# Performance work log

Measured on AMD Instinct MI355X. Metric: run time of the kernel, lower is better.

The kernel has to match this reference:

```python
import jax, jax.numpy as jnp
import numpy as np

B, N, IN_C, HID_C, OUT_C = 8, 2048, 128, 256, 32


def setup_inputs() -> dict:
    key = jax.random.key(0)
    ks = jax.random.split(key, 8)
    s1 = 1.0 / np.sqrt(IN_C)
    s2 = 1.0 / np.sqrt(HID_C)
    return {
        "x": jax.random.normal(ks[0], (B, N, IN_C), dtype=jnp.float32),
        "A": jax.random.randint(ks[1], (B, N, N), 0, 2, dtype=jnp.int32),
        "W1_l": jax.random.normal(ks[2], (IN_C, HID_C), dtype=jnp.float32) * s1,
        "W1_r": jax.random.normal(ks[3], (IN_C, HID_C), dtype=jnp.float32) * s1,
        "b1": jnp.zeros((HID_C,), dtype=jnp.float32),
        "W2_l": jax.random.normal(ks[4], (HID_C, OUT_C), dtype=jnp.float32) * s2,
        "W2_r": jax.random.normal(ks[5], (HID_C, OUT_C), dtype=jnp.float32) * s2,
        "b2": jnp.zeros((OUT_C,), dtype=jnp.float32),
    }


def _mean_agg(mask, deg_inv, h):
    # edge (i, j) means source i -> target j (PyG source_to_target flow):
    # agg[b, j] = mean over i with A[b, i, j] != 0 of h[b, i]
    return jnp.einsum("bij,bid->bjd", mask, h) * deg_inv


def reference(x, A, W1_l, W1_r, b1, W2_l, W2_r, b2):
    mask = (A != 0).astype(x.dtype)            # [B, N, N]
    deg = jnp.sum(mask, axis=1)                # in-degree per target node, [B, N]
    deg_inv = (1.0 / jnp.maximum(deg, 1.0))[..., None]  # isolated nodes -> 0 agg

    # SAGEConv 1: lin_l(mean_agg(x)) + lin_r(x) + bias, then ReLU
    # (dropout p=0.2 is inactive in eval mode)
    h = _mean_agg(mask, deg_inv, x) @ W1_l + x @ W1_r + b1
    h = jax.nn.relu(h)

    # SAGEConv 2
    out = _mean_agg(mask, deg_inv, h) @ W2_l + h @ W2_r + b2  # [B, N, OUT_C]
    return (jax.nn.log_softmax(out, axis=-1), out)
```

## Files before the change

### kernel.cpp

```cpp
#include <hip/hip_runtime.h>


#define B_   8
#define N_   2048
#define INC  128
#define HID  256
#define OUTC 32

typedef __attribute__((ext_vector_type(8))) __bf16 bf16x8;
typedef __attribute__((ext_vector_type(4))) float f32x4;
typedef __attribute__((ext_vector_type(4))) unsigned int u32x4;
typedef __attribute__((ext_vector_type(2))) unsigned int u32x2;

__device__ __forceinline__ unsigned short f2bf(float f) {
  unsigned int u = __float_as_uint(f);
  u += 0x7FFFu + ((u >> 16) & 1u);
  return (unsigned short)(u >> 16);
}

__device__ __forceinline__ f32x4 mfma16(bf16x8 a, bf16x8 b, f32x4 c) {
  return __builtin_amdgcn_mfma_f32_16x16x32_bf16(a, b, c, 0, 0, 0);
}

__device__ __forceinline__ bf16x8 ones_frag() {
  union { unsigned short u[8]; bf16x8 v; } o;
#pragma unroll
  for (int i = 0; i < 8; i++) o.u[i] = 0x3F80;
  return o.v;
}

__device__ __forceinline__ void lut_init(u32x2* lut, int t) {
  if (t < 16) {
    unsigned int w0 = (t & 1 ? 0x3F80u : 0u) | (t & 2 ? 0x3F800000u : 0u);
    unsigned int w1 = (t & 4 ? 0x3F80u : 0u) | (t & 8 ? 0x3F800000u : 0u);
    u32x2 e = {w0, w1};
    lut[t] = e;
  }
}

__device__ __forceinline__ bf16x8 expand8(const u32x2* lut, unsigned int bval) {
  union { u32x2 u2[2]; bf16x8 v; } af;
  af.u2[0] = lut[bval & 15u];
  af.u2[1] = lut[bval >> 4];
  return af.v;
}

__global__ __launch_bounds__(256, 8) void k_prep(
    const int* __restrict__ A, const float* __restrict__ x,
    const float* __restrict__ W1l, const float* __restrict__ W1r,
    const float* __restrict__ W2l, const float* __restrict__ W2r,
    unsigned int* __restrict__ bits, unsigned short* __restrict__ xT,
    unsigned short* __restrict__ xcat,
    unsigned short* __restrict__ W1cT, unsigned short* __restrict__ W2cT) {
  __shared__ unsigned short xls[128 * 72];
  const int bx = blockIdx.x, t = threadIdx.x;
  if (bx < 2048) {
    const int w = t >> 6, l = t & 63;
    const int b = bx & 7, tile4 = bx >> 3;
    const int gw2 = tile4 * 4 + w;
    const int it = gw2 >> 5, jt = gw2 & 31;
    const int i0 = it * 64, j0 = jt * 64;
    const int* Ap = A + ((size_t)(b * N_) + i0) * N_ + j0 + l;
    unsigned long long col = 0;
#pragma unroll 8
    for (int r = 0; r < 64; r++) {
      int a = Ap[(size_t)r * N_];
      unsigned long long m = __ballot(a != 0);
      col |= ((m >> l) & 1ull) << r;
    }
    *reinterpret_cast<unsigned long long*>(
        bits + ((size_t)(b * N_) + j0 + l) * 64 + (i0 >> 5)) = col;
  } else if (bx < 2304) {
    const int bb = bx - 2048;
    const int b = bb & 7, it = bb >> 3;
    const int i0 = it * 64;
    const int dq = (t & 31) * 4;
    const int irow = t >> 5;
#pragma unroll
    for (int s = 0; s < 8; s++) {
      int il = s * 8 + irow;
      int i = i0 + il;
      f32x4 v = *reinterpret_cast<const f32x4*>(x + ((size_t)(b * N_ + i)) * INC + dq);
      unsigned int p0 = f2bf(v[0]) | ((unsigned int)f2bf(v[1]) << 16);
      unsigned int p1 = f2bf(v[2]) | ((unsigned int)f2bf(v[3]) << 16);
      u32x2 pk = {p0, p1};
      *reinterpret_cast<u32x2*>(xcat + ((size_t)(b * N_ + i)) * INC + dq) = pk;
      xls[(dq + 0) * 72 + il] = f2bf(v[0]);
      xls[(dq + 1) * 72 + il] = f2bf(v[1]);
      xls[(dq + 2) * 72 + il] = f2bf(v[2]);
      xls[(dq + 3) * 72 + il] = f2bf(v[3]);
    }
    __syncthreads();
    const int d = t >> 1, half = t & 1;
    const u32x4* src = reinterpret_cast<const u32x4*>(&xls[d * 72 + half * 32]);
    u32x4* dst = reinterpret_cast<u32x4*>(xT + ((size_t)(b * INC + d)) * N_ + i0 + half * 32);
#pragma unroll
    for (int q = 0; q < 4; q++) dst[q] = src[q];
  } else if (bx < 2368) {
    int base = (bx - 2304) * 1024 + t * 4;
#pragma unroll
    for (int q = 0; q < 4; q++) {
      int id = base + q;
      int e = id >> 8, k = id & 255;
      float v = (k < 128) ? W1l[k * 256 + e] : W1r[(k - 128) * 256 + e];
      W1cT[id] = f2bf(v);
    }
  } else {
    int base = (bx - 2368) * 1024 + t * 4;
#pragma unroll
    for (int q = 0; q < 4; q++) {
      int id = base + q;
      int n = id >> 8, k = id & 255;
      float v = (n < 32) ? W2l[k * 32 + n] : W2r[k * 32 + (n - 32)];
      W2cT[id] = f2bf(v);
    }
  }
}

__global__ __launch_bounds__(256, 2) void k_fused1(
    const unsigned int* __restrict__ bits, const unsigned short* __restrict__ xT,
    const unsigned short* __restrict__ xcat,
    const unsigned short* __restrict__ W1cT, const unsigned short* __restrict__ W2cT,
    const float* __restrict__ b1, const float* __restrict__ b2,
    unsigned short* __restrict__ hlT, float* __restrict__ hr,
    float* __restrict__ deg_inv) {
  __shared__ u32x2 lut[16];
  __shared__ __align__(16) float pdeg[4][2][16][4];
  __shared__ __align__(16) unsigned short acat_s[32 * 264];
  union SU {
    float part[4][6][2][64][4];
    unsigned short hs[32 * 264];
  };
  __shared__ __align__(16) SU su;

  const int t = threadIdx.x;
  const int w = t >> 6, l = t & 63, lr = l & 15, lq = l >> 4;
  lut_init(lut, t);

  const int b = blockIdx.x & 7, j0 = (blockIdx.x >> 3) * 32;

  const int xr = t >> 3, xs = t & 7;
  const unsigned short* xp = xcat + ((size_t)(b * N_ + j0 + xr)) * INC + xs * 16;
  u32x4 xpart0 = *reinterpret_cast<const u32x4*>(xp);
  u32x4 xpart1 = *reinterpret_cast<const u32x4*>(xp + 8);

  __syncthreads();

  const unsigned int* bp0 = bits + ((size_t)(b * N_ + j0 + lr)) * 64 + w * 16;
  const unsigned int* bp1 = bp0 + (size_t)16 * 64;
  const unsigned short* xb = xT + (size_t)b * INC * N_ + w * 512;

  const f32x4 zero = {0.f, 0.f, 0.f, 0.f};
  f32x4 acc[2][8];
#pragma unroll
  for (int jt = 0; jt < 2; jt++)
#pragma unroll
    for (int ds = 0; ds < 8; ds++) acc[jt][ds] = zero;
  f32x4 dacc[2] = {zero, zero};
  const bf16x8 onesf = ones_frag();

  for (int s = 0; s < 16; s++) {
    bf16x8 af0 = expand8(lut, (bp0[s] >> (lq * 8)) & 0xFFu);
    bf16x8 af1 = expand8(lut, (bp1[s] >> (lq * 8)) & 0xFFu);
    dacc[0] = mfma16(af0, onesf, dacc[0]);
    dacc[1] = mfma16(af1, onesf, dacc[1]);
#pragma unroll
    for (int ds = 0; ds < 8; ds++) {
      bf16x8 bfr = *reinterpret_cast<const bf16x8*>(
          xb + ((size_t)(ds * 16 + lr)) * N_ + s * 32 + lq * 8);
      acc[0][ds] = mfma16(af0, bfr, acc[0][ds]);
      acc[1][ds] = mfma16(af1, bfr, acc[1][ds]);
    }
  }

#pragma unroll
  for (int ds = 0; ds < 8; ds++) {
    if ((ds >> 1) != w) {
      int dsi = (ds < 2 * w) ? ds : ds - 2;
#pragma unroll
      for (int jt = 0; jt < 2; jt++)
        *reinterpret_cast<f32x4*>(&su.part[w][dsi][jt][l][0]) = acc[jt][ds];
    }
  }
  if (lr == 0) {
#pragma unroll
    for (int jt = 0; jt < 2; jt++)
      *reinterpret_cast<f32x4*>(&pdeg[w][jt][lq][0]) = dacc[jt];
  }
  *reinterpret_cast<u32x4*>(&acat_s[xr * 264 + 128 + xs * 16]) = xpart0;
  *reinterpret_cast<u32x4*>(&acat_s[xr * 264 + 128 + xs * 16 + 8]) = xpart1;
  __syncthreads();

  float dinv2[2][4];
#pragma unroll
  for (int jt = 0; jt < 2; jt++)
#pragma unroll
    for (int r = 0; r < 4; r++) {
      float deg = pdeg[0][jt][lq][r] + pdeg[1][jt][lq][r] +
                  pdeg[2][jt][lq][r] + pdeg[3][jt][lq][r];
      dinv2[jt][r] = 1.0f / fmaxf(deg, 1.0f);
    }
  if (w < 2 && lr == 0) {
#pragma unroll
    for (int r = 0; r < 4; r++)
      deg_inv[b * N_ + j0 + w * 16 + lq * 4 + r] = dinv2[w][r];
  }
#pragma unroll
  for (int dd = 0; dd < 2; dd++) {
    int ds = 2 * w + dd;
#pragma unroll
    for (int jt = 0; jt < 2; jt++) {
      f32x4 sum = acc[jt][ds];
#pragma unroll
      for (int src = 0; src < 4; src++) {
        if (src != w) {
          int dsi = (ds < 2 * src) ? ds : ds - 2;
          f32x4 p = *reinterpret_cast<f32x4*>(&su.part[src][dsi][jt][l][0]);
          sum += p;
        }
      }
#pragma unroll
      for (int r = 0; r < 4; r++)
        acat_s[(jt * 16 + lq * 4 + r) * 264 + ds * 16 + lr] =
            f2bf(sum[r] * dinv2[jt][r]);
    }
  }
  __syncthreads();

  f32x4 acc2[2][4];
#pragma unroll
  for (int jt = 0; jt < 2; jt++)
#pragma unroll
    for (int es = 0; es < 4; es++) acc2[jt][es] = zero;
  const int e0 = w * 64;
#pragma unroll
  for (int ks = 0; ks < 8; ks++) {
    bf16x8 af0 = *reinterpret_cast<const bf16x8*>(&acat_s[lr * 264 + ks * 32 + lq * 8]);
    bf16x8 af1 = *reinterpret_cast<const bf16x8*>(&acat_s[(16 + lr) * 264 + ks * 32 + lq * 8]);
#pragma unroll
    for (int es = 0; es < 4; es++) {
      bf16x8 bfr = *reinterpret_cast<const bf16x8*>(
          W1cT + ((size_t)(e0 + es * 16 + lr)) * HID + ks * 32 + lq * 8);
      acc2[0][es] = mfma16(af0, bfr, acc2[0][es]);
      acc2[1][es] = mfma16(af1, bfr, acc2[1][es]);
    }
  }
  __syncthreads();
#pragma unroll
  for (int jt = 0; jt < 2; jt++)
#pragma unroll
    for (int es = 0; es < 4; es++) {
      int e = e0 + es * 16 + lr;
      float bias = b1[e];
#pragma unroll
      for (int r = 0; r < 4; r++)
        su.hs[(jt * 16 + lq * 4 + r) * 264 + e] =
            f2bf(fmaxf(acc2[jt][es][r] + bias, 0.0f));
    }
  __syncthreads();

  const int jt = w & 1, nh = w >> 1;
  f32x4 a2[2] = {zero, zero};
#pragma unroll
  for (int ks = 0; ks < 8; ks++) {
    bf16x8 af = *reinterpret_cast<const bf16x8*>(
        &su.hs[(jt * 16 + lr) * 264 + ks * 32 + lq * 8]);
#pragma unroll
    for (int ns = 0; ns < 2; ns++) {
      bf16x8 bfr = *reinterpret_cast<const bf16x8*>(
          W2cT + ((size_t)(nh * 32 + ns * 16 + lr)) * HID + ks * 32 + lq * 8);
      a2[ns] = mfma16(af, bfr, a2[ns]);
    }
  }
  if (nh == 0) {
#pragma unroll
    for (int ns = 0; ns < 2; ns++) {
      int c = ns * 16 + lr;
      unsigned int p0 = f2bf(a2[ns][0]) | ((unsigned int)f2bf(a2[ns][1]) << 16);
      unsigned int p1 = f2bf(a2[ns][2]) | ((unsigned int)f2bf(a2[ns][3]) << 16);
      u32x2 pk = {p0, p1};
      *reinterpret_cast<u32x2*>(
          hlT + ((size_t)(b * 32 + c)) * N_ + j0 + jt * 16 + lq * 4) = pk;
    }
  } else {
#pragma unroll
    for (int ns = 0; ns < 2; ns++) {
      int c = ns * 16 + lr;
      float bias = b2[c];
#pragma unroll
      for (int r = 0; r < 4; r++)
        hr[((size_t)(b * N_ + j0 + jt * 16 + lq * 4 + r)) * OUTC + c] = a2[ns][r] + bias;
    }
  }
}

__global__ __launch_bounds__(256, 2) void k_agg2out(
    const unsigned int* __restrict__ bits, const unsigned short* __restrict__ hlT,
    const float* __restrict__ deg_inv, const float* __restrict__ hr,
    float* __restrict__ out) {
  __shared__ u32x2 lut[16];
  __shared__ __align__(16) float part[4][2][2][64][4];
  const int t = threadIdx.x;
  const int w = t >> 6, l = t & 63, lr = l & 15, lq = l >> 4;
  lut_init(lut, t);
  __syncthreads();
  const int b = blockIdx.x & 7, j0 = (blockIdx.x >> 3) * 32;
  const unsigned int* bp0 = bits + ((size_t)(b * N_ + j0 + lr)) * 64 + w * 16;
  const unsigned int* bp1 = bp0 + (size_t)16 * 64;
  const unsigned short* hb = hlT + (size_t)b * 32 * N_ + w * 512;

  const f32x4 zero = {0.f, 0.f, 0.f, 0.f};
  f32x4 acc[2][2] = {{zero, zero}, {zero, zero}};

  for (int s = 0; s < 16; s++) {
    bf16x8 af0 = expand8(lut, (bp0[s] >> (lq * 8)) & 0xFFu);
    bf16x8 af1 = expand8(lut, (bp1[s] >> (lq * 8)) & 0xFFu);
#pragma unroll
    for (int cs = 0; cs < 2; cs++) {
      bf16x8 bfr = *reinterpret_cast<const bf16x8*>(
          hb + ((size_t)(cs * 16 + lr)) * N_ + s * 32 + lq * 8);
      acc[0][cs] = mfma16(af0, bfr, acc[0][cs]);
      acc[1][cs] = mfma16(af1, bfr, acc[1][cs]);
    }
  }
#pragma unroll
  for (int jt = 0; jt < 2; jt++)
#pragma unroll
    for (int cs = 0; cs < 2; cs++)
      *reinterpret_cast<f32x4*>(&part[w][jt][cs][l][0]) = acc[jt][cs];
  __syncthreads();
  if (w >= 2) return;

  const int jt = w;
  const size_t SZ = (size_t)B_ * N_ * OUTC;
#pragma unroll
  for (int r = 0; r < 4; r++) {
    int j = j0 + jt * 16 + lq * 4 + r;
    float dv = deg_inv[b * N_ + j];
    size_t base = ((size_t)(b * N_ + j)) * OUTC;
    float v0 = (part[0][jt][0][l][r] + part[1][jt][0][l][r] +
                part[2][jt][0][l][r] + part[3][jt][0][l][r]) * dv + hr[base + lr];
    float v1 = (part[0][jt][1][l][r] + part[1][jt][1][l][r] +
                part[2][jt][1][l][r] + part[3][jt][1][l][r]) * dv + hr[base + 16 + lr];
    float m = fmaxf(v0, v1);
#pragma unroll
    for (int d = 1; d < 16; d <<= 1) m = fmaxf(m, __shfl_xor(m, d, 64));
    float s = __expf(v0 - m) + __expf(v1 - m);
#pragma unroll
    for (int d = 1; d < 16; d <<= 1) s += __shfl_xor(s, d, 64);
    float ls = m + __logf(s);
    out[base + lr] = v0 - ls;
    out[base + 16 + lr] = v1 - ls;
    out[SZ + base + lr] = v0;
    out[SZ + base + 16 + lr] = v1;
  }
}

extern "C" void kernel_launch(void* const* d_in, const int* in_sizes, int n_in,
                              void* d_out, int out_size, void* d_ws, size_t ws_size,
                              hipStream_t stream) {
  (void)in_sizes; (void)n_in; (void)out_size; (void)ws_size;
  const float* x   = (const float*)d_in[0];
  const int*   A   = (const int*)d_in[1];
  const float* W1l = (const float*)d_in[2];
  const float* W1r = (const float*)d_in[3];
  const float* b1  = (const float*)d_in[4];
  const float* W2l = (const float*)d_in[5];
  const float* W2r = (const float*)d_in[6];
  const float* b2  = (const float*)d_in[7];
  float* out = (float*)d_out;

  char* ws = (char*)d_ws;
  unsigned short* W1cT    = (unsigned short*)(ws + 0);
  unsigned short* W2cT    = (unsigned short*)(ws + 131072);
  float*          deg_inv = (float*)(ws + 163840);
  unsigned int*   bits    = (unsigned int*)(ws + 229376);
  unsigned short* xT      = (unsigned short*)(ws + 4423680);
  unsigned short* xcat    = (unsigned short*)(ws + 8617984);
  unsigned short* hlT     = (unsigned short*)(ws + 12812288);
  float*          hr      = (float*)(ws + 13860864);

  k_prep   <<<dim3(2384), dim3(256), 0, stream>>>(A, x, W1l, W1r, W2l, W2r,
                                                  bits, xT, xcat, W1cT, W2cT);
  k_fused1 <<<dim3(512),  dim3(256), 0, stream>>>(bits, xT, xcat, W1cT, W2cT,
                                                  b1, b2, hlT, hr, deg_inv);
  k_agg2out<<<dim3(512),  dim3(256), 0, stream>>>(bits, hlT, deg_inv, hr, out);
}
```

Baseline: 284.3 us.

## Vectorize adjacency bit-packing and drop xcat intermediate buffer

```diff
diff --git a/kernel.cpp b/kernel.cpp
--- a/kernel.cpp
+++ b/kernel.cpp
@@ -50,28 +50,31 @@
     const float* __restrict__ W1l, const float* __restrict__ W1r,
     const float* __restrict__ W2l, const float* __restrict__ W2r,
     unsigned int* __restrict__ bits, unsigned short* __restrict__ xT,
-    unsigned short* __restrict__ xcat,
     unsigned short* __restrict__ W1cT, unsigned short* __restrict__ W2cT) {
   __shared__ unsigned short xls[128 * 72];
   const int bx = blockIdx.x, t = threadIdx.x;
-  if (bx < 2048) {
+  if (bx < 512) {
     const int w = t >> 6, l = t & 63;
-    const int b = bx & 7, tile4 = bx >> 3;
-    const int gw2 = tile4 * 4 + w;
-    const int it = gw2 >> 5, jt = gw2 & 31;
-    const int i0 = it * 64, j0 = jt * 64;
-    const int* Ap = A + ((size_t)(b * N_) + i0) * N_ + j0 + l;
-    unsigned long long col = 0;
+    const int b = bx & 7, tile = bx >> 3;
+    const int ti = tile >> 3, tj = tile & 7;
+    const int i0 = ti * 256 + w * 64, jc = tj * 256 + 4 * l;
+    const int* Ap = A + ((size_t)(b * N_) + i0) * N_ + jc;
+    unsigned long long cc0 = 0, cc1 = 0, cc2 = 0, cc3 = 0;
 #pragma unroll 8
     for (int r = 0; r < 64; r++) {
-      int a = Ap[(size_t)r * N_];
-      unsigned long long m = __ballot(a != 0);
-      col |= ((m >> l) & 1ull) << r;
-    }
-    *reinterpret_cast<unsigned long long*>(
-        bits + ((size_t)(b * N_) + j0 + l) * 64 + (i0 >> 5)) = col;
-  } else if (bx < 2304) {
-    const int bb = bx - 2048;
+      u32x4 v = *reinterpret_cast<const u32x4*>(Ap + (size_t)r * N_);
+      cc0 |= (unsigned long long)(v[0] != 0u) << r;
+      cc1 |= (unsigned long long)(v[1] != 0u) << r;
+      cc2 |= (unsigned long long)(v[2] != 0u) << r;
+      cc3 |= (unsigned long long)(v[3] != 0u) << r;
+    }
+    unsigned int* bp = bits + ((size_t)(b * N_) + jc) * 64 + (i0 >> 5);
+    *reinterpret_cast<unsigned long long*>(bp) = cc0;
+    *reinterpret_cast<unsigned long long*>(bp + 64) = cc1;
+    *reinterpret_cast<unsigned long long*>(bp + 128) = cc2;
+    *reinterpret_cast<unsigned long long*>(bp + 192) = cc3;
+  } else if (bx < 768) {
+    const int bb = bx - 512;
     const int b = bb & 7, it = bb >> 3;
     const int i0 = it * 64;
     const int dq = (t & 31) * 4;
@@ -81,10 +84,6 @@
       int il = s * 8 + irow;
       int i = i0 + il;
       f32x4 v = *reinterpret_cast<const f32x4*>(x + ((size_t)(b * N_ + i)) * INC + dq);
-      unsigned int p0 = f2bf(v[0]) | ((unsigned int)f2bf(v[1]) << 16);
-      unsigned int p1 = f2bf(v[2]) | ((unsigned int)f2bf(v[3]) << 16);
-      u32x2 pk = {p0, p1};
-      *reinterpret_cast<u32x2*>(xcat + ((size_t)(b * N_ + i)) * INC + dq) = pk;
       xls[(dq + 0) * 72 + il] = f2bf(v[0]);
       xls[(dq + 1) * 72 + il] = f2bf(v[1]);
       xls[(dq + 2) * 72 + il] = f2bf(v[2]);
@@ -96,8 +95,8 @@
     u32x4* dst = reinterpret_cast<u32x4*>(xT + ((size_t)(b * INC + d)) * N_ + i0 + half * 32);
 #pragma unroll
     for (int q = 0; q < 4; q++) dst[q] = src[q];
-  } else if (bx < 2368) {
-    int base = (bx - 2304) * 1024 + t * 4;
+  } else if (bx < 832) {
+    int base = (bx - 768) * 1024 + t * 4;
 #pragma unroll
     for (int q = 0; q < 4; q++) {
       int id = base + q;
@@ -106,7 +105,7 @@
       W1cT[id] = f2bf(v);
     }
   } else {
-    int base = (bx - 2368) * 1024 + t * 4;
+    int base = (bx - 832) * 1024 + t * 4;
 #pragma unroll
     for (int q = 0; q < 4; q++) {
       int id = base + q;
@@ -119,7 +118,7 @@
 
 __global__ __launch_bounds__(256, 2) void k_fused1(
     const unsigned int* __restrict__ bits, const unsigned short* __restrict__ xT,
-    const unsigned short* __restrict__ xcat,
+    const float* __restrict__ x,
     const unsigned short* __restrict__ W1cT, const unsigned short* __restrict__ W2cT,
     const float* __restrict__ b1, const float* __restrict__ b2,
     unsigned short* __restrict__ hlT, float* __restrict__ hr,
@@ -139,10 +138,11 @@
 
   const int b = blockIdx.x & 7, j0 = (blockIdx.x >> 3) * 32;
 
-  const int xr = t >> 3, xs = t & 7;
-  const unsigned short* xp = xcat + ((size_t)(b * N_ + j0 + xr)) * INC + xs * 16;
-  u32x4 xpart0 = *reinterpret_cast<const u32x4*>(xp);
-  u32x4 xpart1 = *reinterpret_cast<const u32x4*>(xp + 8);
+  const int xr = t >> 3, xq = (t & 7) * 16;
+  const float* xp = x + ((size_t)(b * N_ + j0 + xr)) * INC + xq;
+  f32x4 xv[4];
+#pragma unroll
+  for (int q = 0; q < 4; q++) xv[q] = *reinterpret_cast<const f32x4*>(xp + q * 4);
 
   __syncthreads();
 
@@ -187,8 +187,13 @@
     for (int jt = 0; jt < 2; jt++)
       *reinterpret_cast<f32x4*>(&pdeg[w][jt][lq][0]) = dacc[jt];
   }
-  *reinterpret_cast<u32x4*>(&acat_s[xr * 264 + 128 + xs * 16]) = xpart0;
-  *reinterpret_cast<u32x4*>(&acat_s[xr * 264 + 128 + xs * 16 + 8]) = xpart1;
+#pragma unroll
+  for (int q = 0; q < 4; q++) {
+    unsigned int p0 = f2bf(xv[q][0]) | ((unsigned int)f2bf(xv[q][1]) << 16);
+    unsigned int p1 = f2bf(xv[q][2]) | ((unsigned int)f2bf(xv[q][3]) << 16);
+    u32x2 pk = {p0, p1};
+    *reinterpret_cast<u32x2*>(&acat_s[xr * 264 + 128 + xq + q * 4]) = pk;
+  }
   __syncthreads();
 
   float dinv2[2][4];
@@ -376,13 +381,12 @@
   float*          deg_inv = (float*)(ws + 163840);
   unsigned int*   bits    = (unsigned int*)(ws + 229376);
   unsigned short* xT      = (unsigned short*)(ws + 4423680);
-  unsigned short* xcat    = (unsigned short*)(ws + 8617984);
-  unsigned short* hlT     = (unsigned short*)(ws + 12812288);
-  float*          hr      = (float*)(ws + 13860864);
-
-  k_prep   <<<dim3(2384), dim3(256), 0, stream>>>(A, x, W1l, W1r, W2l, W2r,
-                                                  bits, xT, xcat, W1cT, W2cT);
-  k_fused1 <<<dim3(512),  dim3(256), 0, stream>>>(bits, xT, xcat, W1cT, W2cT,
-                                                  b1, b2, hlT, hr, deg_inv);
-  k_agg2out<<<dim3(512),  dim3(256), 0, stream>>>(bits, hlT, deg_inv, hr, out);
-}
+  unsigned short* hlT     = (unsigned short*)(ws + 8617984);
+  float*          hr      = (float*)(ws + 9666560);
+
+  k_prep   <<<dim3(848), dim3(256), 0, stream>>>(A, x, W1l, W1r, W2l, W2r,
+                                                 bits, xT, W1cT, W2cT);
+  k_fused1 <<<dim3(512), dim3(256), 0, stream>>>(bits, xT, x, W1cT, W2cT,
+                                                 b1, b2, hlT, hr, deg_inv);
+  k_agg2out<<<dim3(512), dim3(256), 0, stream>>>(bits, hlT, deg_inv, hr, out);
+}
```

New measurement: 284.9 us. About the same (+0.2%).
